# Performance work log

Hardware: AMD Instinct MI355X
Metric: run time of the kernel (lower is better)

The kernel has to match this reference:

```python
import jax, jax.numpy as jnp
import numpy as np

N, D_IN, D_HID, D_OUT = 16384, 512, 2048, 512
NUM_BANDS, RANK, ALPHA = 4, 16, 32
SCALING = ALPHA / RANK  # 2.0


def setup_inputs() -> dict:
    key = jax.random.key(0)
    ks = jax.random.split(key, 10)
    x = jax.random.normal(ks[0], (N, D_IN), dtype=jnp.float32)
    bw = jax.random.uniform(ks[1], (N, NUM_BANDS), dtype=jnp.float32)
    band_weights = bw / jnp.sum(bw, axis=-1, keepdims=True)  # rows sum to 1
    s_in = 1.0 / np.sqrt(D_IN)
    s_hid = 1.0 / np.sqrt(D_HID)
    return {
        "x": x,
        "band_weights": band_weights,
        "W1": jax.random.normal(ks[2], (D_IN, D_HID), dtype=jnp.float32) * s_in,
        "b1": jax.random.normal(ks[3], (D_HID,), dtype=jnp.float32) * 0.01,
        "W2": jax.random.normal(ks[4], (D_HID, D_OUT), dtype=jnp.float32) * s_hid,
        "b2": jax.random.normal(ks[5], (D_OUT,), dtype=jnp.float32) * 0.01,
        "lora_fc1_A": jax.random.normal(ks[6], (NUM_BANDS, D_IN, RANK), dtype=jnp.float32) * s_in,
        "lora_fc1_B": jax.random.normal(ks[7], (NUM_BANDS, RANK, D_HID), dtype=jnp.float32) * 0.02,
        "lora_fc2_A": jax.random.normal(ks[8], (NUM_BANDS, D_HID, RANK), dtype=jnp.float32) * s_hid,
        "lora_fc2_B": jax.random.normal(ks[9], (NUM_BANDS, RANK, D_OUT), dtype=jnp.float32) * 0.02,
    }


def reference(x, band_weights, W1, b1, W2, b2, lora_fc1_A, lora_fc1_B, lora_fc2_A, lora_fc2_B):
    # shared fc1: [N, hidden]
    h_shared = x @ W1 + b1
    # per-band LoRA down-projection: [N, bands, rank]
    t1 = jnp.einsum('ni,bir->nbr', x, lora_fc1_A)
    # up-project and band-weighted sum fused: [N, hidden]
    delta1 = jnp.einsum('nb,nbr,brh->nh', band_weights, t1, lora_fc1_B) * SCALING
    h = jax.nn.gelu(h_shared + delta1, approximate=False)  # torch GELU is erf-based
    out_shared = h @ W2 + b2
    t2 = jnp.einsum('nh,bhr->nbr', h, lora_fc2_A)
    delta2 = jnp.einsum('nb,nbr,bro->no', band_weights, t2, lora_fc2_B) * SCALING
    return out_shared + delta2
```

## Files before the change

### kernel.cpp

```cpp
#include <hip/hip_runtime.h>
#include <hip/hip_bf16.h>

#define DEV __device__ __forceinline__
#define AS1 __attribute__((address_space(1)))
#define AS3 __attribute__((address_space(3)))

typedef __attribute__((ext_vector_type(8))) short bf16x8;
typedef __attribute__((ext_vector_type(4))) float f32x4;

static constexpr int NR   = 16384;
static constexpr int DIN  = 512;
static constexpr int DHID = 2048;
static constexpr int DOUT = 512;
static constexpr int LR   = 64;
static constexpr int K1   = DIN + LR;
static constexpr int K2   = DHID + LR;

DEV unsigned short f2bf(float f) {
  unsigned u = __float_as_uint(f);
  u += 0x7fffu + ((u >> 16) & 1u);
  return (unsigned short)(u >> 16);
}

DEV float fast_gelu(float v) {
  float x2 = v * v;
  float a  = -v * __builtin_fmaf(0.10294324f, x2, 2.30220817f);
  float t  = exp2f(a);
  return v * __builtin_amdgcn_rcpf(1.0f + t);
}

template<int N> DEV void wvm() {
  asm volatile("s_waitcnt vmcnt(%0)" :: "i"(N) : "memory");
}

__global__ __launch_bounds__(256) void cvt_x_kernel(const float* __restrict__ x,
                                                    unsigned short* __restrict__ xaug) {
  int i = blockIdx.x * 256 + threadIdx.x;
  if (i >= NR * DIN / 4) return;
  int e = i * 4;
  int r = e >> 9, c = e & 511;
  float4 v = ((const float4*)x)[i];
  uint2 o;
  o.x = (unsigned)f2bf(v.x) | ((unsigned)f2bf(v.y) << 16);
  o.y = (unsigned)f2bf(v.z) | ((unsigned)f2bf(v.w) << 16);
  *(uint2*)(xaug + (size_t)r * K1 + c) = o;
}

template<int R, int C, int LDO, int CO>
__global__ __launch_bounds__(256) void tconv_kernel(const float* __restrict__ in,
                                                    unsigned short* __restrict__ out) {
  __shared__ float t[32][33];
  int bc = blockIdx.x * 32, br = blockIdx.y * 32;
  int tx = threadIdx.x & 31, ty = threadIdx.x >> 5;
  #pragma unroll
  for (int i = 0; i < 32; i += 8)
    t[ty + i][tx] = in[(size_t)(br + ty + i) * C + bc + tx];
  __syncthreads();
  #pragma unroll
  for (int i = 0; i < 32; i += 8)
    out[(size_t)(bc + ty + i) * LDO + CO + br + tx] = f2bf(t[tx][ty + i]);
}

__global__ __launch_bounds__(256) void rearrA_kernel(const float* __restrict__ A,
                                                     unsigned short* __restrict__ AT, int D) {
  int tid = blockIdx.x * 256 + threadIdx.x;
  if (tid >= 64 * D) return;
  int j = tid / D, i = tid - j * D;
  AT[tid] = f2bf(A[((size_t)(j >> 4) * D + i) * 16 + (j & 15)]);
}

template<int BM, int BN, int WAVES, int K, int EPI>
__global__ __launch_bounds__(WAVES * 64, 2) void gemmx_kernel(
    const unsigned short* __restrict__ A, int lda,
    const unsigned short* __restrict__ B, int ldb,
    const float* __restrict__ bias,
    void* __restrict__ outp, int ldo, int ocol) {
  constexpr int THREADS = WAVES * 64;
  constexpr int NT = K / 64;
  constexpr int AL = BM * 4 / THREADS;
  constexpr int BL = BN * 4 / THREADS;
  constexpr int HA = (BM / 2) * 64;
  constexpr int HB = (BN / 2) * 64;
  constexpr int MQ = BM / 64;
  constexpr int WC = WAVES / 2;
  static_assert(NT >= 2 && AL == 2 && BL == 2, "geometry");
  __shared__ __align__(16) unsigned short lA[4 * HA];
  __shared__ __align__(16) unsigned short lB[4 * HB];

  const int tid  = threadIdx.x;
  const int w    = tid >> 6, lane = tid & 63;
  const int wr   = w / WC, wc = w % WC;
  const int bm   = blockIdx.x * BM, bn = blockIdx.y * BN;
  const int l15  = lane & 15;
  const int kc0  = ((lane >> 4) ^ (lane & 7)) * 8;
  const int kc1  = (((lane >> 4) + 4) ^ (lane & 7)) * 8;

  f32x4 acc[2][2][MQ][2] = {};
  bf16x8 af[2][MQ][2];
  bf16x8 bfv[2][2];

  auto stageA = [&](int buf, int half, int t) {
    #pragma unroll
    for (int i = 0; i < AL; ++i) {
      int row = w * (AL * 8) + i * 8 + (lane >> 3);
      __builtin_amdgcn_global_load_lds(
          (const AS1 void*)(A + (size_t)(bm + half * (BM / 2) + row) * lda
                              + (size_t)t * 64 + (((lane & 7) ^ (row & 7)) * 8)),
          (AS3 void*)(lA + (buf * 2 + half) * HA + (w * AL + i) * 512),
          16, 0, 0);
    }
  };
  auto stageB = [&](int buf, int half, int t) {
    #pragma unroll
    for (int i = 0; i < BL; ++i) {
      int row = w * (BL * 8) + i * 8 + (lane >> 3);
      __builtin_amdgcn_global_load_lds(
          (const AS1 void*)(B + (size_t)(bn + half * (BN / 2) + row) * ldb
                              + (size_t)t * 64 + (((lane & 7) ^ (row & 7)) * 8)),
          (AS3 void*)(lB + (buf * 2 + half) * HB + (w * BL + i) * 512),
          16, 0, 0);
    }
  };
  auto ldAall = [&](int buf) {
    #pragma unroll
    for (int mh = 0; mh < 2; ++mh) {
      const unsigned short* sA = lA + (buf * 2 + mh) * HA;
      #pragma unroll
      for (int m = 0; m < MQ; ++m) {
        int ro = (wr * (BM / 4) + m * 16 + l15) * 64;
        af[mh][m][0] = *(const bf16x8*)(sA + ro + kc0);
        af[mh][m][1] = *(const bf16x8*)(sA + ro + kc1);
      }
    }
  };
  auto ldB = [&](int buf, int nh) {
    const unsigned short* sB = lB + (buf * 2 + nh) * HB;
    #pragma unroll
    for (int n = 0; n < 2; ++n) {
      int ro = (wc * 32 + n * 16 + l15) * 64;
      bfv[n][0] = *(const bf16x8*)(sB + ro + kc0);
      bfv[n][1] = *(const bf16x8*)(sB + ro + kc1);
    }
  };

#define MFMA_Q(mh, nh)                                                           \
  __builtin_amdgcn_s_setprio(1);                                                 \
  _Pragma("unroll")                                                              \
  for (int m = 0; m < MQ; ++m)                                                   \
    _Pragma("unroll")                                                            \
    for (int n = 0; n < 2; ++n) {                                                \
      acc[mh][nh][m][n] = __builtin_amdgcn_mfma_f32_16x16x32_bf16(               \
          af[mh][m][0], bfv[n][0], acc[mh][nh][m][n], 0, 0, 0);                  \
      acc[mh][nh][m][n] = __builtin_amdgcn_mfma_f32_16x16x32_bf16(               \
          af[mh][m][1], bfv[n][1], acc[mh][nh][m][n], 0, 0, 0);                  \
    }                                                                            \
  __builtin_amdgcn_s_setprio(0);

#define BAR() __builtin_amdgcn_s_barrier()

  stageA(0, 0, 0); stageA(0, 1, 0); stageB(0, 0, 0); stageB(0, 1, 0);
  wvm<2>();
  BAR();

  for (int t = 0; t < NT; ++t) {
    const int buf = t & 1, nb = buf ^ 1;
    const bool more = (t + 1 < NT);
    ldAall(buf);
    ldB(buf, 0);
    if (more) { stageA(nb, 0, t + 1); stageA(nb, 1, t + 1); stageB(nb, 0, t + 1); }
    MFMA_Q(0, 0);
    MFMA_Q(1, 0);
    if (more) wvm<6>(); else wvm<0>();
    BAR();
    if (more) stageB(nb, 1, t + 1);
    ldB(buf, 1);
    MFMA_Q(0, 1);
    MFMA_Q(1, 1);
    if (more) {
      wvm<2>();
      BAR();
    }
  }
#undef MFMA_Q
#undef BAR

  float biasv[2][2];
  #pragma unroll
  for (int nh = 0; nh < 2; ++nh)
    #pragma unroll
    for (int n = 0; n < 2; ++n)
      biasv[nh][n] = bias[bn + nh * (BN / 2) + wc * 32 + n * 16 + l15];

  #pragma unroll
  for (int mh = 0; mh < 2; ++mh)
    #pragma unroll
    for (int nh = 0; nh < 2; ++nh)
      #pragma unroll
      for (int m = 0; m < MQ; ++m)
        #pragma unroll
        for (int n = 0; n < 2; ++n) {
          int col  = bn + nh * (BN / 2) + wc * 32 + n * 16 + l15;
          int rowb = bm + mh * (BM / 2) + wr * (BM / 4) + m * 16 + ((lane >> 4) << 2);
          #pragma unroll
          for (int r = 0; r < 4; ++r) {
            float v = acc[mh][nh][m][n][r];
            int row = rowb + r;
            if (EPI == 0) {
              v = fast_gelu(v + biasv[nh][n]);
              ((unsigned short*)outp)[(size_t)row * ldo + ocol + col] = f2bf(v);
            } else {
              v += biasv[nh][n];
              ((float*)outp)[(size_t)row * ldo + col] = v;
            }
          }
        }
}

template<int BM, int BN, int WM, int WN, int K>
__global__ __launch_bounds__(256) void gemmu_kernel(
    const unsigned short* __restrict__ A, int lda,
    const unsigned short* __restrict__ B, int ldb,
    const float* __restrict__ bw,
    unsigned short* __restrict__ outp, int ldo, int ocol) {
  constexpr int WRM = WM / 16, WRN = WN / 16;
  constexpr int NWN = BN / WN;
  constexpr int NT  = K / 64;
  constexpr int NBUF = 3;
  constexpr int AISS = BM * 64 * 2 / 4096;
  constexpr int BISS = BN * 64 * 2 / 4096;
  constexpr int LOADS = AISS + BISS;
  static_assert((BM / WM) * (BN / WN) == 4 && NT >= NBUF, "geometry");
  __shared__ __align__(16) unsigned short lA[NBUF * BM * 64];
  __shared__ __align__(16) unsigned short lB[NBUF * BN * 64];

  const int tid  = threadIdx.x;
  const int wid  = tid >> 6, lane = tid & 63;
  const int wr   = wid / NWN, wc = wid % NWN;
  const int bm   = blockIdx.x * BM, bn = blockIdx.y * BN;
  const int l15  = lane & 15;
  const int kc0  = ((lane >> 4) ^ (lane & 7)) * 8;
  const int kc1  = (((lane >> 4) + 4) ^ (lane & 7)) * 8;

  f32x4 acc[WRM][WRN] = {};

  auto stage = [&](int buf, int t) {
    #pragma unroll
    for (int i = 0; i < AISS; i++) {
      int row = (wid * AISS + i) * 8 + (lane >> 3);
      __builtin_amdgcn_global_load_lds(
          (const AS1 void*)(A + (size_t)(bm + row) * lda + (size_t)t * 64
                              + (((lane & 7) ^ (row & 7)) * 8)),
          (AS3 void*)(lA + buf * (BM * 64) + (wid * AISS + i) * 512), 16, 0, 0);
    }
    #pragma unroll
    for (int i = 0; i < BISS; i++) {
      int row = (wid * BISS + i) * 8 + (lane >> 3);
      __builtin_amdgcn_global_load_lds(
          (const AS1 void*)(B + (size_t)(bn + row) * ldb + (size_t)t * 64
                              + (((lane & 7) ^ (row & 7)) * 8)),
          (AS3 void*)(lB + buf * (BN * 64) + (wid * BISS + i) * 512), 16, 0, 0);
    }
  };
  auto compute = [&](int buf) {
    const unsigned short* pA = lA + buf * (BM * 64);
    const unsigned short* pB = lB + buf * (BN * 64);
    bf16x8 af[WRM][2], bfv[WRN][2];
    #pragma unroll
    for (int m = 0; m < WRM; m++) {
      int ro = (wr * WM + m * 16 + l15) * 64;
      af[m][0] = *(const bf16x8*)(pA + ro + kc0);
      af[m][1] = *(const bf16x8*)(pA + ro + kc1);
    }
    #pragma unroll
    for (int n = 0; n < WRN; n++) {
      int ro = (wc * WN + n * 16 + l15) * 64;
      bfv[n][0] = *(const bf16x8*)(pB + ro + kc0);
      bfv[n][1] = *(const bf16x8*)(pB + ro + kc1);
    }
    #pragma unroll
    for (int m = 0; m < WRM; m++)
      #pragma unroll
      for (int n = 0; n < WRN; n++) {
        acc[m][n] = __builtin_amdgcn_mfma_f32_16x16x32_bf16(af[m][0], bfv[n][0], acc[m][n], 0, 0, 0);
        acc[m][n] = __builtin_amdgcn_mfma_f32_16x16x32_bf16(af[m][1], bfv[n][1], acc[m][n], 0, 0, 0);
      }
  };

  stage(0, 0); stage(1, 1); stage(2, 2);
  wvm<2 * LOADS>();
  __builtin_amdgcn_s_barrier();

  int bt = 0;
  for (int t = 0; t < NT; ++t) {
    compute(bt);
    __builtin_amdgcn_s_barrier();
    if (t + 1 < NT) {
      if (t + NBUF < NT) stage(bt, t + NBUF);
      int newer = (t + NBUF < NT) ? (NBUF - 1) : (NT - 2 - t);
      if (newer >= 2)      wvm<2 * LOADS>();
      else if (newer == 1) wvm<LOADS>();
      else                 wvm<0>();
      __builtin_amdgcn_s_barrier();
      bt = (bt == NBUF - 1) ? 0 : bt + 1;
    }
  }

  const int r0 = bm + wr * WM;
  const int c0 = bn + wc * WN;
  #pragma unroll
  for (int m = 0; m < WRM; m++)
    #pragma unroll
    for (int n = 0; n < WRN; n++) {
      int col  = c0 + n * 16 + l15;
      int rowb = r0 + m * 16 + ((lane >> 4) << 2);
      #pragma unroll
      for (int r = 0; r < 4; r++) {
        float v = acc[m][n][r] * 2.0f * bw[(rowb + r) * 4 + (col >> 4)];
        outp[(size_t)(rowb + r) * ldo + ocol + col] = f2bf(v);
      }
    }
}

extern "C" void kernel_launch(void* const* d_in, const int* in_sizes, int n_in,
                              void* d_out, int out_size, void* d_ws, size_t ws_size,
                              hipStream_t stream) {
  const float* x  = (const float*)d_in[0];
  const float* bw = (const float*)d_in[1];
  const float* W1 = (const float*)d_in[2];
  const float* b1 = (const float*)d_in[3];
  const float* W2 = (const float*)d_in[4];
  const float* b2 = (const float*)d_in[5];
  const float* A1 = (const float*)d_in[6];
  const float* B1 = (const float*)d_in[7];
  const float* A2 = (const float*)d_in[8];
  const float* B2 = (const float*)d_in[9];
  float* out = (float*)d_out;

  char* w = (char*)d_ws;
  unsigned short* xaug = (unsigned short*)w;  w += (size_t)NR * K1 * 2;
  unsigned short* haug = (unsigned short*)w;  w += (size_t)NR * K2 * 2;
  unsigned short* W1cT = (unsigned short*)w;  w += (size_t)DHID * K1 * 2;
  unsigned short* W2cT = (unsigned short*)w;  w += (size_t)DOUT * K2 * 2;
  unsigned short* A1T  = (unsigned short*)w;  w += (size_t)64 * DIN * 2;
  unsigned short* A2T  = (unsigned short*)w;  w += (size_t)64 * DHID * 2;

  cvt_x_kernel<<<NR * DIN / 4 / 256, 256, 0, stream>>>(x, xaug);
  tconv_kernel<512, 2048, K1, 0><<<dim3(64, 16), 256, 0, stream>>>(W1, W1cT);
  tconv_kernel<64, 2048, K1, 512><<<dim3(64, 2), 256, 0, stream>>>(B1, W1cT);
  tconv_kernel<2048, 512, K2, 0><<<dim3(16, 64), 256, 0, stream>>>(W2, W2cT);
  tconv_kernel<64, 512, K2, 2048><<<dim3(16, 2), 256, 0, stream>>>(B2, W2cT);
  rearrA_kernel<<<128, 256, 0, stream>>>(A1, A1T, 512);
  rearrA_kernel<<<512, 256, 0, stream>>>(A2, A2T, 2048);

  gemmu_kernel<64, 64, 32, 32, 512><<<dim3(NR / 64, 1), 256, 0, stream>>>(
      xaug, K1, A1T, DIN, bw, xaug, K1, 512);
  gemmx_kernel<256, 256, 8, K1, 0><<<dim3(NR / 256, DHID / 256), 512, 0, stream>>>(
      xaug, K1, W1cT, K1, b1, haug, K2, 0);
  gemmu_kernel<64, 64, 32, 32, 2048><<<dim3(NR / 64, 1), 256, 0, stream>>>(
      haug, K2, A2T, DHID, bw, haug, K2, 2048);
  gemmx_kernel<128, 128, 4, K2, 1><<<dim3(NR / 128, DOUT / 128), 256, 0, stream>>>(
      haug, K2, W2cT, K2, b2, out, DOUT, 0);
}
```

Baseline: 145.0 us.

## Replace pipelined double-buffered GEMM with simple single-buffer 4-wave GEMM

```diff
diff --git a/kernel.cpp b/kernel.cpp
--- a/kernel.cpp
+++ b/kernel.cpp
@@ -69,151 +69,99 @@
   AT[tid] = f2bf(A[((size_t)(j >> 4) * D + i) * 16 + (j & 15)]);
 }
 
-template<int BM, int BN, int WAVES, int K, int EPI>
-__global__ __launch_bounds__(WAVES * 64, 2) void gemmx_kernel(
+template<int BM, int BN, int WM, int WN, int K, int EPI>
+__global__ __launch_bounds__(256) void gemm97_kernel(
     const unsigned short* __restrict__ A, int lda,
     const unsigned short* __restrict__ B, int ldb,
     const float* __restrict__ bias,
     void* __restrict__ outp, int ldo, int ocol) {
-  constexpr int THREADS = WAVES * 64;
-  constexpr int NT = K / 64;
-  constexpr int AL = BM * 4 / THREADS;
-  constexpr int BL = BN * 4 / THREADS;
-  constexpr int HA = (BM / 2) * 64;
-  constexpr int HB = (BN / 2) * 64;
-  constexpr int MQ = BM / 64;
-  constexpr int WC = WAVES / 2;
-  static_assert(NT >= 2 && AL == 2 && BL == 2, "geometry");
-  __shared__ __align__(16) unsigned short lA[4 * HA];
-  __shared__ __align__(16) unsigned short lB[4 * HB];
+  constexpr int NT   = K / 64;
+  constexpr int AISS = BM / 32;
+  constexpr int BISS = BN / 32;
+  constexpr int WRM  = WM / 16, WRN = WN / 16;
+  static_assert((BM / WM) * (BN / WN) == 4, "4 waves");
+  __shared__ __align__(16) unsigned short lA[BM * 64];
+  __shared__ __align__(16) unsigned short lB[BN * 64];
 
   const int tid  = threadIdx.x;
   const int w    = tid >> 6, lane = tid & 63;
-  const int wr   = w / WC, wc = w % WC;
+  const int wr   = w >> 1, wc = w & 1;
   const int bm   = blockIdx.x * BM, bn = blockIdx.y * BN;
   const int l15  = lane & 15;
+  const int srow = lane >> 3;
   const int kc0  = ((lane >> 4) ^ (lane & 7)) * 8;
   const int kc1  = (((lane >> 4) + 4) ^ (lane & 7)) * 8;
 
-  f32x4 acc[2][2][MQ][2] = {};
-  bf16x8 af[2][MQ][2];
-  bf16x8 bfv[2][2];
-
-  auto stageA = [&](int buf, int half, int t) {
-    #pragma unroll
-    for (int i = 0; i < AL; ++i) {
-      int row = w * (AL * 8) + i * 8 + (lane >> 3);
+  f32x4 acc[WRM][WRN] = {};
+
+  for (int t = 0; t < NT; ++t) {
+    #pragma unroll
+    for (int i = 0; i < AISS; ++i) {
+      int row = i * 32 + w * 8 + srow;
       __builtin_amdgcn_global_load_lds(
-          (const AS1 void*)(A + (size_t)(bm + half * (BM / 2) + row) * lda
-                              + (size_t)t * 64 + (((lane & 7) ^ (row & 7)) * 8)),
-          (AS3 void*)(lA + (buf * 2 + half) * HA + (w * AL + i) * 512),
-          16, 0, 0);
-    }
-  };
-  auto stageB = [&](int buf, int half, int t) {
-    #pragma unroll
-    for (int i = 0; i < BL; ++i) {
-      int row = w * (BL * 8) + i * 8 + (lane >> 3);
+          (const AS1 void*)(A + (size_t)(bm + row) * lda + (size_t)t * 64
+                              + (((lane & 7) ^ (row & 7)) * 8)),
+          (AS3 void*)(lA + (i * 32 + w * 8) * 64 + lane * 8), 16, 0, 0);
+    }
+    #pragma unroll
+    for (int i = 0; i < BISS; ++i) {
+      int row = i * 32 + w * 8 + srow;
       __builtin_amdgcn_global_load_lds(
-          (const AS1 void*)(B + (size_t)(bn + half * (BN / 2) + row) * ldb
-                              + (size_t)t * 64 + (((lane & 7) ^ (row & 7)) * 8)),
-          (AS3 void*)(lB + (buf * 2 + half) * HB + (w * BL + i) * 512),
-          16, 0, 0);
-    }
-  };
-  auto ldAall = [&](int buf) {
-    #pragma unroll
-    for (int mh = 0; mh < 2; ++mh) {
-      const unsigned short* sA = lA + (buf * 2 + mh) * HA;
+          (const AS1 void*)(B + (size_t)(bn + row) * ldb + (size_t)t * 64
+                              + (((lane & 7) ^ (row & 7)) * 8)),
+          (AS3 void*)(lB + (i * 32 + w * 8) * 64 + lane * 8), 16, 0, 0);
+    }
+    __syncthreads();
+
+    bf16x8 af[WRM][2], bfv[WRN][2];
+    #pragma unroll
+    for (int m = 0; m < WRM; ++m) {
+      int ro = (wr * WM + m * 16 + l15) * 64;
+      af[m][0] = *(const bf16x8*)(lA + ro + kc0);
+      af[m][1] = *(const bf16x8*)(lA + ro + kc1);
+    }
+    #pragma unroll
+    for (int n = 0; n < WRN; ++n) {
+      int ro = (wc * WN + n * 16 + l15) * 64;
+      bfv[n][0] = *(const bf16x8*)(lB + ro + kc0);
+      bfv[n][1] = *(const bf16x8*)(lB + ro + kc1);
+    }
+    #pragma unroll
+    for (int m = 0; m < WRM; ++m)
       #pragma unroll
-      for (int m = 0; m < MQ; ++m) {
-        int ro = (wr * (BM / 4) + m * 16 + l15) * 64;
-        af[mh][m][0] = *(const bf16x8*)(sA + ro + kc0);
-        af[mh][m][1] = *(const bf16x8*)(sA + ro + kc1);
+      for (int n = 0; n < WRN; ++n) {
+        acc[m][n] = __builtin_amdgcn_mfma_f32_16x16x32_bf16(af[m][0], bfv[n][0], acc[m][n], 0, 0, 0);
+        acc[m][n] = __builtin_amdgcn_mfma_f32_16x16x32_bf16(af[m][1], bfv[n][1], acc[m][n], 0, 0, 0);
       }
-    }
-  };
-  auto ldB = [&](int buf, int nh) {
-    const unsigned short* sB = lB + (buf * 2 + nh) * HB;
-    #pragma unroll
-    for (int n = 0; n < 2; ++n) {
-      int ro = (wc * 32 + n * 16 + l15) * 64;
-      bfv[n][0] = *(const bf16x8*)(sB + ro + kc0);
-      bfv[n][1] = *(const bf16x8*)(sB + ro + kc1);
-    }
-  };
-
-#define MFMA_Q(mh, nh)                                                           \
-  __builtin_amdgcn_s_setprio(1);                                                 \
-  _Pragma("unroll")                                                              \
-  for (int m = 0; m < MQ; ++m)                                                   \
-    _Pragma("unroll")                                                            \
-    for (int n = 0; n < 2; ++n) {                                                \
-      acc[mh][nh][m][n] = __builtin_amdgcn_mfma_f32_16x16x32_bf16(               \
-          af[mh][m][0], bfv[n][0], acc[mh][nh][m][n], 0, 0, 0);                  \
-      acc[mh][nh][m][n] = __builtin_amdgcn_mfma_f32_16x16x32_bf16(               \
-          af[mh][m][1], bfv[n][1], acc[mh][nh][m][n], 0, 0, 0);                  \
-    }                                                                            \
-  __builtin_amdgcn_s_setprio(0);
-
-#define BAR() __builtin_amdgcn_s_barrier()
-
-  stageA(0, 0, 0); stageA(0, 1, 0); stageB(0, 0, 0); stageB(0, 1, 0);
-  wvm<2>();
-  BAR();
-
-  for (int t = 0; t < NT; ++t) {
-    const int buf = t & 1, nb = buf ^ 1;
-    const bool more = (t + 1 < NT);
-    ldAall(buf);
-    ldB(buf, 0);
-    if (more) { stageA(nb, 0, t + 1); stageA(nb, 1, t + 1); stageB(nb, 0, t + 1); }
-    MFMA_Q(0, 0);
-    MFMA_Q(1, 0);
-    if (more) wvm<6>(); else wvm<0>();
-    BAR();
-    if (more) stageB(nb, 1, t + 1);
-    ldB(buf, 1);
-    MFMA_Q(0, 1);
-    MFMA_Q(1, 1);
-    if (more) {
-      wvm<2>();
-      BAR();
-    }
+    __syncthreads();
   }
-#undef MFMA_Q
-#undef BAR
-
-  float biasv[2][2];
-  #pragma unroll
-  for (int nh = 0; nh < 2; ++nh)
-    #pragma unroll
-    for (int n = 0; n < 2; ++n)
-      biasv[nh][n] = bias[bn + nh * (BN / 2) + wc * 32 + n * 16 + l15];
-
-  #pragma unroll
-  for (int mh = 0; mh < 2; ++mh)
-    #pragma unroll
-    for (int nh = 0; nh < 2; ++nh)
+
+  const int r0 = bm + wr * WM;
+  const int c0 = bn + wc * WN;
+  float biasv[WRN];
+  #pragma unroll
+  for (int n = 0; n < WRN; ++n)
+    biasv[n] = bias[c0 + n * 16 + l15];
+
+  #pragma unroll
+  for (int m = 0; m < WRM; ++m)
+    #pragma unroll
+    for (int n = 0; n < WRN; ++n) {
+      int col  = c0 + n * 16 + l15;
+      int rowb = r0 + m * 16 + ((lane >> 4) << 2);
       #pragma unroll
-      for (int m = 0; m < MQ; ++m)
-        #pragma unroll
-        for (int n = 0; n < 2; ++n) {
-          int col  = bn + nh * (BN / 2) + wc * 32 + n * 16 + l15;
-          int rowb = bm + mh * (BM / 2) + wr * (BM / 4) + m * 16 + ((lane >> 4) << 2);
-          #pragma unroll
-          for (int r = 0; r < 4; ++r) {
-            float v = acc[mh][nh][m][n][r];
-            int row = rowb + r;
-            if (EPI == 0) {
-              v = fast_gelu(v + biasv[nh][n]);
-              ((unsigned short*)outp)[(size_t)row * ldo + ocol + col] = f2bf(v);
-            } else {
-              v += biasv[nh][n];
-              ((float*)outp)[(size_t)row * ldo + col] = v;
-            }
-          }
+      for (int r = 0; r < 4; ++r) {
+        float v = acc[m][n][r];
+        int row = rowb + r;
+        if (EPI == 0) {
+          v = fast_gelu(v + biasv[n]);
+          ((unsigned short*)outp)[(size_t)row * ldo + ocol + col] = f2bf(v);
+        } else {
+          v += biasv[n];
+          ((float*)outp)[(size_t)row * ldo + col] = v;
         }
+      }
+    }
 }
 
 template<int BM, int BN, int WM, int WN, int K>
@@ -354,10 +302,10 @@
 
   gemmu_kernel<64, 64, 32, 32, 512><<<dim3(NR / 64, 1), 256, 0, stream>>>(
       xaug, K1, A1T, DIN, bw, xaug, K1, 512);
-  gemmx_kernel<256, 256, 8, K1, 0><<<dim3(NR / 256, DHID / 256), 512, 0, stream>>>(
+  gemm97_kernel<128, 256, 64, 128, K1, 0><<<dim3(NR / 128, DHID / 256), 256, 0, stream>>>(
       xaug, K1, W1cT, K1, b1, haug, K2, 0);
   gemmu_kernel<64, 64, 32, 32, 2048><<<dim3(NR / 64, 1), 256, 0, stream>>>(
       haug, K2, A2T, DHID, bw, haug, K2, 2048);
-  gemmx_kernel<128, 128, 4, K2, 1><<<dim3(NR / 128, DOUT / 128), 256, 0, stream>>>(
+  gemm97_kernel<64, 128, 32, 64, K2, 1><<<dim3(NR / 64, DOUT / 128), 256, 0, stream>>>(
       haug, K2, W2cT, K2, b2, out, DOUT, 0);
 }
```

Result: slower. 187.9 us (+29.6%).

## Switch big GEMMs to 32x32x16 MFMA and merge prep kernels into one launch

Applied to the files above, without the earlier changes.

```diff
diff --git a/kernel.cpp b/kernel.cpp
--- a/kernel.cpp
+++ b/kernel.cpp
@@ -7,6 +7,7 @@
 
 typedef __attribute__((ext_vector_type(8))) short bf16x8;
 typedef __attribute__((ext_vector_type(4))) float f32x4;
+typedef __attribute__((ext_vector_type(16))) float f32x16;
 
 static constexpr int NR   = 16384;
 static constexpr int DIN  = 512;
@@ -33,25 +34,10 @@
   asm volatile("s_waitcnt vmcnt(%0)" :: "i"(N) : "memory");
 }
 
-__global__ __launch_bounds__(256) void cvt_x_kernel(const float* __restrict__ x,
-                                                    unsigned short* __restrict__ xaug) {
-  int i = blockIdx.x * 256 + threadIdx.x;
-  if (i >= NR * DIN / 4) return;
-  int e = i * 4;
-  int r = e >> 9, c = e & 511;
-  float4 v = ((const float4*)x)[i];
-  uint2 o;
-  o.x = (unsigned)f2bf(v.x) | ((unsigned)f2bf(v.y) << 16);
-  o.y = (unsigned)f2bf(v.z) | ((unsigned)f2bf(v.w) << 16);
-  *(uint2*)(xaug + (size_t)r * K1 + c) = o;
-}
-
-template<int R, int C, int LDO, int CO>
-__global__ __launch_bounds__(256) void tconv_kernel(const float* __restrict__ in,
-                                                    unsigned short* __restrict__ out) {
-  __shared__ float t[32][33];
-  int bc = blockIdx.x * 32, br = blockIdx.y * 32;
-  int tx = threadIdx.x & 31, ty = threadIdx.x >> 5;
+DEV void tconv_dev(const float* in, unsigned short* out, int C, int LDO, int CO,
+                   int bx, int by, float (*t)[33], int tid) {
+  int bc = bx * 32, br = by * 32;
+  int tx = tid & 31, ty = tid >> 5;
   #pragma unroll
   for (int i = 0; i < 32; i += 8)
     t[ty + i][tx] = in[(size_t)(br + ty + i) * C + bc + tx];
@@ -61,16 +47,49 @@
     out[(size_t)(bc + ty + i) * LDO + CO + br + tx] = f2bf(t[tx][ty + i]);
 }
 
-__global__ __launch_bounds__(256) void rearrA_kernel(const float* __restrict__ A,
-                                                     unsigned short* __restrict__ AT, int D) {
-  int tid = blockIdx.x * 256 + threadIdx.x;
-  if (tid >= 64 * D) return;
-  int j = tid / D, i = tid - j * D;
-  AT[tid] = f2bf(A[((size_t)(j >> 4) * D + i) * 16 + (j & 15)]);
+__global__ __launch_bounds__(256) void prep_kernel(
+    const float* __restrict__ x, unsigned short* __restrict__ xaug,
+    const float* __restrict__ W1, const float* __restrict__ B1,
+    const float* __restrict__ W2, const float* __restrict__ B2,
+    unsigned short* __restrict__ W1cT, unsigned short* __restrict__ W2cT,
+    const float* __restrict__ A1, const float* __restrict__ A2,
+    unsigned short* __restrict__ A1T, unsigned short* __restrict__ A2T) {
+  __shared__ float t[32][33];
+  const int b = blockIdx.x, tid = threadIdx.x;
+  if (b < 8192) {
+    int i = b * 256 + tid;
+    int e = i * 4;
+    int r = e >> 9, c = e & 511;
+    float4 v = ((const float4*)x)[i];
+    uint2 o;
+    o.x = (unsigned)f2bf(v.x) | ((unsigned)f2bf(v.y) << 16);
+    o.y = (unsigned)f2bf(v.z) | ((unsigned)f2bf(v.w) << 16);
+    *(uint2*)(xaug + (size_t)r * K1 + c) = o;
+  } else if (b < 9216) {
+    int bi = b - 8192;
+    tconv_dev(W1, W1cT, 2048, K1, 0, bi & 63, bi >> 6, t, tid);
+  } else if (b < 10240) {
+    int bi = b - 9216;
+    tconv_dev(W2, W2cT, 512, K2, 0, bi & 15, bi >> 4, t, tid);
+  } else if (b < 10368) {
+    int bi = b - 10240;
+    tconv_dev(B1, W1cT, 2048, K1, 512, bi & 63, bi >> 6, t, tid);
+  } else if (b < 10400) {
+    int bi = b - 10368;
+    tconv_dev(B2, W2cT, 512, K2, 2048, bi & 15, bi >> 4, t, tid);
+  } else if (b < 10528) {
+    int i2 = (b - 10400) * 256 + tid;
+    int j = i2 / DIN, i = i2 - j * DIN;
+    A1T[i2] = f2bf(A1[((size_t)(j >> 4) * DIN + i) * 16 + (j & 15)]);
+  } else {
+    int i2 = (b - 10528) * 256 + tid;
+    int j = i2 / DHID, i = i2 - j * DHID;
+    A2T[i2] = f2bf(A2[((size_t)(j >> 4) * DHID + i) * 16 + (j & 15)]);
+  }
 }
 
 template<int BM, int BN, int WAVES, int K, int EPI>
-__global__ __launch_bounds__(WAVES * 64, 2) void gemmx_kernel(
+__global__ __launch_bounds__(WAVES * 64, 2) void gemm32_kernel(
     const unsigned short* __restrict__ A, int lda,
     const unsigned short* __restrict__ B, int ldb,
     const float* __restrict__ bias,
@@ -81,9 +100,9 @@
   constexpr int BL = BN * 4 / THREADS;
   constexpr int HA = (BM / 2) * 64;
   constexpr int HB = (BN / 2) * 64;
-  constexpr int MQ = BM / 64;
+  constexpr int MH = BM / 128;
   constexpr int WC = WAVES / 2;
-  static_assert(NT >= 2 && AL == 2 && BL == 2, "geometry");
+  static_assert(NT >= 2 && AL == 2 && BL == 2 && (BN / 2) / WC == 32, "geometry");
   __shared__ __align__(16) unsigned short lA[4 * HA];
   __shared__ __align__(16) unsigned short lB[4 * HB];
 
@@ -91,13 +110,13 @@
   const int w    = tid >> 6, lane = tid & 63;
   const int wr   = w / WC, wc = w % WC;
   const int bm   = blockIdx.x * BM, bn = blockIdx.y * BN;
-  const int l15  = lane & 15;
-  const int kc0  = ((lane >> 4) ^ (lane & 7)) * 8;
-  const int kc1  = (((lane >> 4) + 4) ^ (lane & 7)) * 8;
-
-  f32x4 acc[2][2][MQ][2] = {};
-  bf16x8 af[2][MQ][2];
-  bf16x8 bfv[2][2];
+  const int l31  = lane & 31;
+  const int kh   = lane >> 5;
+  const int swz  = lane & 7;
+
+  f32x16 acc[2][2][MH] = {};
+  bf16x8 af[2][MH][4];
+  bf16x8 bfv[4];
 
   auto stageA = [&](int buf, int half, int t) {
     #pragma unroll
@@ -126,34 +145,32 @@
     for (int mh = 0; mh < 2; ++mh) {
       const unsigned short* sA = lA + (buf * 2 + mh) * HA;
       #pragma unroll
-      for (int m = 0; m < MQ; ++m) {
-        int ro = (wr * (BM / 4) + m * 16 + l15) * 64;
-        af[mh][m][0] = *(const bf16x8*)(sA + ro + kc0);
-        af[mh][m][1] = *(const bf16x8*)(sA + ro + kc1);
+      for (int m = 0; m < MH; ++m) {
+        int ro = (wr * (BM / 4) + m * 32 + l31) * 64;
+        #pragma unroll
+        for (int ks = 0; ks < 4; ++ks)
+          af[mh][m][ks] = *(const bf16x8*)(sA + ro + (((2 * ks + kh) ^ swz) * 8));
       }
     }
   };
   auto ldB = [&](int buf, int nh) {
     const unsigned short* sB = lB + (buf * 2 + nh) * HB;
-    #pragma unroll
-    for (int n = 0; n < 2; ++n) {
-      int ro = (wc * 32 + n * 16 + l15) * 64;
-      bfv[n][0] = *(const bf16x8*)(sB + ro + kc0);
-      bfv[n][1] = *(const bf16x8*)(sB + ro + kc1);
-    }
-  };
-
-#define MFMA_Q(mh, nh)                                                           \
+    int ro = (wc * 32 + l31) * 64;
+    #pragma unroll
+    for (int ks = 0; ks < 4; ++ks)
+      bfv[ks] = *(const bf16x8*)(sB + ro + (((2 * ks + kh) ^ swz) * 8));
+  };
+
+#define MFMA_C(nh)                                                               \
   __builtin_amdgcn_s_setprio(1);                                                 \
   _Pragma("unroll")                                                              \
-  for (int m = 0; m < MQ; ++m)                                                   \
+  for (int mh = 0; mh < 2; ++mh)                                                 \
     _Pragma("unroll")                                                            \
-    for (int n = 0; n < 2; ++n) {                                                \
-      acc[mh][nh][m][n] = __builtin_amdgcn_mfma_f32_16x16x32_bf16(               \
-          af[mh][m][0], bfv[n][0], acc[mh][nh][m][n], 0, 0, 0);                  \
-      acc[mh][nh][m][n] = __builtin_amdgcn_mfma_f32_16x16x32_bf16(               \
-          af[mh][m][1], bfv[n][1], acc[mh][nh][m][n], 0, 0, 0);                  \
-    }                                                                            \
+    for (int m = 0; m < MH; ++m)                                                 \
+      _Pragma("unroll")                                                          \
+      for (int ks = 0; ks < 4; ++ks)                                             \
+        acc[mh][nh][m] = __builtin_amdgcn_mfma_f32_32x32x16_bf16(                \
+            af[mh][m][ks], bfv[ks], acc[mh][nh][m], 0, 0, 0);                    \
   __builtin_amdgcn_s_setprio(0);
 
 #define BAR() __builtin_amdgcn_s_barrier()
@@ -168,52 +185,46 @@
     ldAall(buf);
     ldB(buf, 0);
     if (more) { stageA(nb, 0, t + 1); stageA(nb, 1, t + 1); stageB(nb, 0, t + 1); }
-    MFMA_Q(0, 0);
-    MFMA_Q(1, 0);
+    MFMA_C(0);
     if (more) wvm<6>(); else wvm<0>();
     BAR();
     if (more) stageB(nb, 1, t + 1);
     ldB(buf, 1);
-    MFMA_Q(0, 1);
-    MFMA_Q(1, 1);
+    MFMA_C(1);
     if (more) {
       wvm<2>();
       BAR();
     }
   }
-#undef MFMA_Q
+#undef MFMA_C
 #undef BAR
 
-  float biasv[2][2];
+  float biasv[2];
   #pragma unroll
   for (int nh = 0; nh < 2; ++nh)
-    #pragma unroll
-    for (int n = 0; n < 2; ++n)
-      biasv[nh][n] = bias[bn + nh * (BN / 2) + wc * 32 + n * 16 + l15];
+    biasv[nh] = bias[bn + nh * (BN / 2) + wc * 32 + l31];
 
   #pragma unroll
   for (int mh = 0; mh < 2; ++mh)
     #pragma unroll
     for (int nh = 0; nh < 2; ++nh)
       #pragma unroll
-      for (int m = 0; m < MQ; ++m)
+      for (int m = 0; m < MH; ++m) {
+        int col  = bn + nh * (BN / 2) + wc * 32 + l31;
+        int rowb = bm + mh * (BM / 2) + wr * (BM / 4) + m * 32 + 4 * (lane >> 5);
         #pragma unroll
-        for (int n = 0; n < 2; ++n) {
-          int col  = bn + nh * (BN / 2) + wc * 32 + n * 16 + l15;
-          int rowb = bm + mh * (BM / 2) + wr * (BM / 4) + m * 16 + ((lane >> 4) << 2);
-          #pragma unroll
-          for (int r = 0; r < 4; ++r) {
-            float v = acc[mh][nh][m][n][r];
-            int row = rowb + r;
-            if (EPI == 0) {
-              v = fast_gelu(v + biasv[nh][n]);
-              ((unsigned short*)outp)[(size_t)row * ldo + ocol + col] = f2bf(v);
-            } else {
-              v += biasv[nh][n];
-              ((float*)outp)[(size_t)row * ldo + col] = v;
-            }
+        for (int r = 0; r < 16; ++r) {
+          float v = acc[mh][nh][m][r];
+          int row = rowb + (r & 3) + 8 * (r >> 2);
+          if (EPI == 0) {
+            v = fast_gelu(v + biasv[nh]);
+            ((unsigned short*)outp)[(size_t)row * ldo + ocol + col] = f2bf(v);
+          } else {
+            v += biasv[nh];
+            ((float*)outp)[(size_t)row * ldo + col] = v;
           }
         }
+      }
 }
 
 template<int BM, int BN, int WM, int WN, int K>
@@ -344,20 +355,15 @@
   unsigned short* A1T  = (unsigned short*)w;  w += (size_t)64 * DIN * 2;
   unsigned short* A2T  = (unsigned short*)w;  w += (size_t)64 * DHID * 2;
 
-  cvt_x_kernel<<<NR * DIN / 4 / 256, 256, 0, stream>>>(x, xaug);
-  tconv_kernel<512, 2048, K1, 0><<<dim3(64, 16), 256, 0, stream>>>(W1, W1cT);
-  tconv_kernel<64, 2048, K1, 512><<<dim3(64, 2), 256, 0, stream>>>(B1, W1cT);
-  tconv_kernel<2048, 512, K2, 0><<<dim3(16, 64), 256, 0, stream>>>(W2, W2cT);
-  tconv_kernel<64, 512, K2, 2048><<<dim3(16, 2), 256, 0, stream>>>(B2, W2cT);
-  rearrA_kernel<<<128, 256, 0, stream>>>(A1, A1T, 512);
-  rearrA_kernel<<<512, 256, 0, stream>>>(A2, A2T, 2048);
+  prep_kernel<<<11040, 256, 0, stream>>>(x, xaug, W1, B1, W2, B2,
+                                         W1cT, W2cT, A1, A2, A1T, A2T);
 
   gemmu_kernel<64, 64, 32, 32, 512><<<dim3(NR / 64, 1), 256, 0, stream>>>(
       xaug, K1, A1T, DIN, bw, xaug, K1, 512);
-  gemmx_kernel<256, 256, 8, K1, 0><<<dim3(NR / 256, DHID / 256), 512, 0, stream>>>(
+  gemm32_kernel<256, 256, 8, K1, 0><<<dim3(NR / 256, DHID / 256), 512, 0, stream>>>(
       xaug, K1, W1cT, K1, b1, haug, K2, 0);
   gemmu_kernel<64, 64, 32, 32, 2048><<<dim3(NR / 64, 1), 256, 0, stream>>>(
       haug, K2, A2T, DHID, bw, haug, K2, 2048);
-  gemmx_kernel<128, 128, 4, K2, 1><<<dim3(NR / 128, DOUT / 128), 256, 0, stream>>>(
+  gemm32_kernel<128, 128, 4, K2, 1><<<dim3(NR / 128, DOUT / 128), 256, 0, stream>>>(
       haug, K2, W2cT, K2, b2, out, DOUT, 0);
 }
```

New measurement: 144.2 us. No clear change (-0.6%).
